# Kernel tuning notes

Measured on AMD Instinct MI355X. Metric: run time of the kernel, lower is better.

## Reference

```python
import jax, jax.numpy as jnp
import numpy as np

LRELU_ALPHA = 0.2
ACT_GAIN = float(np.sqrt(2.0))  # def_gain for 'lrelu' in StyleGAN2 bias_act


def setup_inputs() -> dict:
    key = jax.random.key(0)
    k_x, k_w, k_aw, k_wt = jax.random.split(key, 4)
    N, C_in, C_out, H, W, Wdim, K = 8, 256, 256, 128, 128, 512, 3
    x = jax.random.normal(k_x, (N, C_in, H, W), dtype=jnp.float32)
    w = jax.random.normal(k_w, (N, Wdim), dtype=jnp.float32)
    # FullyConnectedLayer params: weight ~ randn([out, in]) (lr_mult=1), bias_init=1
    affine_w = jax.random.normal(k_aw, (C_in, Wdim), dtype=jnp.float32)
    affine_b = jnp.ones((C_in,), dtype=jnp.float32)
    # Conv weight ~ randn, bias zeros
    weight = jax.random.normal(k_wt, (C_out, C_in, K, K), dtype=jnp.float32)
    bias = jnp.zeros((C_out,), dtype=jnp.float32)
    return {"x": x, "w": w, "affine_w": affine_w, "affine_b": affine_b,
            "weight": weight, "bias": bias}


def reference(x, w, affine_w, affine_b, weight, bias):
    N, C_in, H, W = x.shape
    C_out, _, K, _ = weight.shape
    # affine: runtime weight gain = 1/sqrt(in_features)
    wg = 1.0 / np.sqrt(affine_w.shape[1])
    styles = w @ (affine_w.T * wg) + affine_b                      # [N, C_in]
    # modulate: per-sample weights [N, C_out, C_in, K, K]
    ww = weight[None] * styles[:, None, :, None, None]
    # demodulate
    d = jax.lax.rsqrt(jnp.sum(ww * ww, axis=(2, 3, 4)) + 1e-8)     # [N, C_out]
    ww = ww * d[:, :, None, None, None]
    # fused per-sample conv via grouped conv (groups = N), flip_weight=True -> correlation
    x2 = x.reshape(1, N * C_in, H, W)
    wk = ww.reshape(N * C_out, C_in, K, K)
    pad = K // 2
    out = jax.lax.conv_general_dilated(
        x2, wk, window_strides=(1, 1), padding=((pad, pad), (pad, pad)),
        dimension_numbers=("NCHW", "OIHW", "NCHW"), feature_group_count=N)
    out = out.reshape(N, C_out, H, W)
    # bias_act: lrelu with def_gain sqrt(2), gain=1, no clamp; then sigmoid
    out = out + bias[None, :, None, None]
    out = jnp.where(out >= 0, out, LRELU_ALPHA * out) * ACT_GAIN
    return jax.nn.sigmoid(out)
```

## Files before the change

### kernel.cpp

```cpp
#include <hip/hip_runtime.h>
#include <hip/hip_bf16.h>

typedef __attribute__((ext_vector_type(8))) short bf16x8;
typedef __attribute__((ext_vector_type(4))) float f32x4;
typedef unsigned short ushort_t;

__device__ __forceinline__ void gload16(const void* g, void* l) {
  __builtin_amdgcn_global_load_lds(
      (const __attribute__((address_space(1))) void*)g,
      (__attribute__((address_space(3))) void*)l, 16, 0, 0);
}

__global__ void k_styles(const float* __restrict__ w, const float* __restrict__ aw,
                         const float* __restrict__ ab, float* __restrict__ styles) {
  int wave = threadIdx.x >> 6, l = threadIdx.x & 63;
  int id = blockIdx.x * 4 + wave;
  int n = id >> 8, ci = id & 255;
  const float4* ar = (const float4*)(aw + (size_t)ci * 512);
  const float4* wr = (const float4*)(w + n * 512);
  float s = 0.f;
  #pragma unroll
  for (int j = 0; j < 2; j++) {
    float4 a = ar[l * 2 + j], b = wr[l * 2 + j];
    s += a.x * b.x + a.y * b.y + a.z * b.z + a.w * b.w;
  }
  #pragma unroll
  for (int off = 32; off; off >>= 1) s += __shfl_xor(s, off, 64);
  if (l == 0) styles[n * 256 + ci] = s * 0.044194173824159216f + ab[ci];
}

__global__ __launch_bounds__(256) void k_modw(const float* __restrict__ weight,
                                              const float* __restrict__ styles,
                                              ushort_t* __restrict__ wwg) {
  __shared__ float wl[4][2304];
  __shared__ float s_sty[256];
  int wave = threadIdx.x >> 6, l = threadIdx.x & 63;
  int id = blockIdx.x * 4 + wave;
  int n = id >> 8, co = id & 255;
  s_sty[threadIdx.x] = styles[(size_t)n * 256 + threadIdx.x];
  __syncthreads();
  const float* wrow = weight + (size_t)co * 2304;
  float sq = 0.f;
  #pragma unroll
  for (int i = 0; i < 36; i++) {
    int idx = i * 64 + l;
    float v = wrow[idx] * s_sty[idx / 9];
    sq += v * v;
    wl[wave][idx] = v;
  }
  #pragma unroll
  for (int off = 32; off; off >>= 1) sq += __shfl_xor(sq, off, 64);
  float d = rsqrtf(sq + 1e-8f);
  #pragma unroll
  for (int tap = 0; tap < 9; tap++) {
    int kh = tap / 3, kw = tap % 3;
    #pragma unroll
    for (int cg = 0; cg < 4; cg++) {
      int ci = cg * 64 + l;
      float v = wl[wave][ci * 9 + tap] * d;
      __hip_bfloat16 hb = __float2bfloat16(v);
      size_t oidx = ((((size_t)((n * 3 + kh) * 8) + (ci >> 5)) * 3 + kw) * 256 + co) * 32 + (ci & 31);
      wwg[oidx] = *reinterpret_cast<ushort_t*>(&hb);
    }
  }
}

__global__ void k_transpose(const float* __restrict__ x, ushort_t* __restrict__ xt) {
  int n = blockIdx.z, h = blockIdx.y;
  int wt = blockIdx.x & 1, ct = blockIdx.x >> 1;
  int w0 = wt * 64, ci0 = ct * 64;
  __shared__ float tile[64][68];
  int t = threadIdx.x;
  {
    int ci_l = t >> 2, wq = (t & 3) * 16;
    const float* src = x + (((size_t)(n * 256 + ci0 + ci_l) * 128 + h) * 128 + w0 + wq);
    #pragma unroll
    for (int j = 0; j < 4; j++)
      *(float4*)&tile[ci_l][wq + j * 4] = ((const float4*)src)[j];
  }
  __syncthreads();
  {
    int w_l = t >> 2, cq = (t & 3) * 16;
    union { ushort_t u[16]; uint4 v[2]; } pk;
    #pragma unroll
    for (int j = 0; j < 16; j++) {
      __hip_bfloat16 hb = __float2bfloat16(tile[cq + j][w_l]);
      pk.u[j] = *reinterpret_cast<ushort_t*>(&hb);
    }
    size_t off = ((size_t)((n * 128 + h) * 128) + w0 + w_l) * 256 + ci0 + cq;
    uint4* dst = (uint4*)(xt + off);
    dst[0] = pk.v[0];
    dst[1] = pk.v[1];
  }
}

__global__ __launch_bounds__(256, 2) void k_conv(
    const ushort_t* __restrict__ xt, const ushort_t* __restrict__ wwg,
    const float* __restrict__ bias, float* __restrict__ out) {
  __shared__ __align__(16) char smem[24576 + 2 * 8448];
  char* sA = smem;
  char* sB = smem + 24576;

  const int bid = blockIdx.x;
  const int n  = bid & 7;
  const int r  = bid >> 3;
  const int cb = r & 1;
  const int h0 = (r >> 1) * 2;

  const int t = threadIdx.x;
  const int wave = t >> 6;
  const int l = t & 63;
  const int wr = wave >> 1, wc = wave & 1;
  const int c = l & 15, kg = l >> 4;

  f32x4 acc[4][8];
  #pragma unroll
  for (int i = 0; i < 4; i++)
    #pragma unroll
    for (int j = 0; j < 8; j++)
      acc[i][j] = (f32x4){0.f, 0.f, 0.f, 0.f};

  if (t < 64) {
    int buf = t >> 5;
    int rr = t & 31;
    if (rr < 16) {
      int rowsel = rr >> 2;
      int row = (rowsel == 0) ? 0 : (128 + rowsel);
      *(f32x4*)(sB + buf * 8448 + row * 64 + (rr & 3) * 16) = (f32x4){0.f, 0.f, 0.f, 0.f};
    }
  }

  const long long xtN = (long long)n * (128LL * 128 * 256);

  for (int kh = 0; kh < 3; kh++) {
    const int hsrc_w = h0 + wc + kh - 1;
    const bool valid = (hsrc_w >= 0) && (hsrc_w < 128);
    const char* gAkh = (const char*)(wwg + ((size_t)(n * 3 + kh)) * (8 * 3 * 256 * 32));
    for (int cc = 0; cc < 8; cc++) {
      __syncthreads();
      const char* gA = gAkh + (size_t)cc * (3 * 256 * 32 * 2);
      #pragma unroll
      for (int i = 0; i < 6; i++) {
        int G = i * 256 + t;
        int kw = G >> 9, rr = G & 511;
        const char* gp = gA + kw * 16384 + cb * 8192 + rr * 16;
        char* lp = sA + (i * 256 + wave * 64) * 16;
        gload16(gp, lp);
      }
      #pragma unroll
      for (int i = 0; i < 4; i++) {
        int G = i * 256 + t;
        int rr = G & 511;
        int w = rr >> 2, gg = rr & 3;
        int buf = G >> 9;
        int hsrc = h0 + kh - 1 + buf;
        const char* gp = (const char*)xt +
            ((xtN + (long long)(hsrc * 128 + w) * 256 + cc * 32 + gg * 8) * 2);
        int B0 = i * 256 + wave * 64;
        char* lp = sB + (B0 >> 9) * 8448 + 64 + (B0 & 511) * 16;
        gload16(gp, lp);
      }
      asm volatile("s_waitcnt vmcnt(0)" ::: "memory");
      __syncthreads();
      if (valid) {
        const char* bBase = sB + wc * 8448;
        #pragma unroll
        for (int s = 0; s < 3; s++) {
          bf16x8 af[4];
          #pragma unroll
          for (int mi = 0; mi < 4; mi++)
            af[mi] = *(const bf16x8*)(sA + s * 8192 + (wr * 64 + mi * 16 + c) * 64 + kg * 16);
          bf16x8 bfr[8];
          #pragma unroll
          for (int ni = 0; ni < 8; ni++)
            bfr[ni] = *(const bf16x8*)(bBase + (ni * 16 + c + s) * 64 + kg * 16);
          #pragma unroll
          for (int mi = 0; mi < 4; mi++)
            #pragma unroll
            for (int ni = 0; ni < 8; ni++)
              acc[mi][ni] = __builtin_amdgcn_mfma_f32_16x16x32_bf16(af[mi], bfr[ni], acc[mi][ni], 0, 0, 0);
        }
      }
    }
  }

  const int hrow = h0 + wc;
  #pragma unroll
  for (int mi = 0; mi < 4; mi++) {
    #pragma unroll
    for (int rr = 0; rr < 4; rr++) {
      int co = cb * 128 + wr * 64 + mi * 16 + kg * 4 + rr;
      float bval = bias[co];
      #pragma unroll
      for (int ni = 0; ni < 8; ni++) {
        float v = acc[mi][ni][rr] + bval;
        v = (v >= 0.f ? v : 0.2f * v) * 1.41421356237f;
        float o = 1.f / (1.f + __expf(-v));
        out[(((size_t)(n * 256 + co)) * 128 + hrow) * 128 + ni * 16 + c] = o;
      }
    }
  }
}

extern "C" void kernel_launch(void* const* d_in, const int* in_sizes, int n_in,
                              void* d_out, int out_size, void* d_ws, size_t ws_size,
                              hipStream_t stream) {
  const float* x      = (const float*)d_in[0];
  const float* w      = (const float*)d_in[1];
  const float* aw     = (const float*)d_in[2];
  const float* ab     = (const float*)d_in[3];
  const float* weight = (const float*)d_in[4];
  const float* bias   = (const float*)d_in[5];
  float* out = (float*)d_out;

  char* ws = (char*)d_ws;
  float*    styles = (float*)ws;
  ushort_t* wwg    = (ushort_t*)(ws + 8192);
  ushort_t* xt     = (ushort_t*)(ws + 8192 + 9437184);

  k_styles<<<512, 256, 0, stream>>>(w, aw, ab, styles);
  k_modw<<<512, 256, 0, stream>>>(weight, styles, wwg);
  k_transpose<<<dim3(8, 128, 8), 256, 0, stream>>>(x, xt);
  k_conv<<<1024, 256, 0, stream>>>(xt, wwg, bias, out);
}
```

Measured before the change: 377.2 us.

## Double-buffer conv stages, one output row per block, skip padded kh rows

Restructures the conv kernel so each block computes a single output row (each wave owns 32 output channels), which doubles the grid. Global-to-LDS loads for the next (kh, channel-chunk) stage are issued before computing the current one, using double-buffered LDS. Boundary rows skip the kh iterations that fall entirely in padding instead of loading and then masking them. The trade-off is that weight tiles are reloaded twice as often per output row, and LDS use per block roughly doubles, which may limit occupancy.

Measured after the change: 396.8 us. 1.05x slower.

```diff
diff --git a/kernel.cpp b/kernel.cpp
--- a/kernel.cpp
+++ b/kernel.cpp
@@ -97,106 +97,103 @@
 __global__ __launch_bounds__(256, 2) void k_conv(
     const ushort_t* __restrict__ xt, const ushort_t* __restrict__ wwg,
     const float* __restrict__ bias, float* __restrict__ out) {
-  __shared__ __align__(16) char smem[24576 + 2 * 8448];
-  char* sA = smem;
-  char* sB = smem + 24576;
+  __shared__ __align__(16) char smem[2 * 24576 + 2 * 8448];
 
   const int bid = blockIdx.x;
   const int n  = bid & 7;
   const int r  = bid >> 3;
   const int cb = r & 1;
-  const int h0 = (r >> 1) * 2;
+  const int h0 = r >> 1;
 
   const int t = threadIdx.x;
   const int wave = t >> 6;
   const int l = t & 63;
-  const int wr = wave >> 1, wc = wave & 1;
+  const int wr = wave;
   const int c = l & 15, kg = l >> 4;
 
-  f32x4 acc[4][8];
-  #pragma unroll
-  for (int i = 0; i < 4; i++)
+  f32x4 acc[2][8];
+  #pragma unroll
+  for (int i = 0; i < 2; i++)
     #pragma unroll
     for (int j = 0; j < 8; j++)
       acc[i][j] = (f32x4){0.f, 0.f, 0.f, 0.f};
 
-  if (t < 64) {
-    int buf = t >> 5;
-    int rr = t & 31;
-    if (rr < 16) {
-      int rowsel = rr >> 2;
-      int row = (rowsel == 0) ? 0 : (128 + rowsel);
-      *(f32x4*)(sB + buf * 8448 + row * 64 + (rr & 3) * 16) = (f32x4){0.f, 0.f, 0.f, 0.f};
-    }
+  if (t < 16) {
+    int buf = t >> 3, q = t & 7;
+    int slot = (q >> 2) ? 129 : 0;
+    *(f32x4*)(smem + 49152 + buf * 8448 + slot * 64 + (q & 3) * 16) =
+        (f32x4){0.f, 0.f, 0.f, 0.f};
   }
 
   const long long xtN = (long long)n * (128LL * 128 * 256);
-
-  for (int kh = 0; kh < 3; kh++) {
-    const int hsrc_w = h0 + wc + kh - 1;
-    const bool valid = (hsrc_w >= 0) && (hsrc_w < 128);
-    const char* gAkh = (const char*)(wwg + ((size_t)(n * 3 + kh)) * (8 * 3 * 256 * 32));
-    for (int cc = 0; cc < 8; cc++) {
-      __syncthreads();
-      const char* gA = gAkh + (size_t)cc * (3 * 256 * 32 * 2);
-      #pragma unroll
-      for (int i = 0; i < 6; i++) {
-        int G = i * 256 + t;
-        int kw = G >> 9, rr = G & 511;
-        const char* gp = gA + kw * 16384 + cb * 8192 + rr * 16;
-        char* lp = sA + (i * 256 + wave * 64) * 16;
-        gload16(gp, lp);
-      }
-      #pragma unroll
-      for (int i = 0; i < 4; i++) {
-        int G = i * 256 + t;
-        int rr = G & 511;
-        int w = rr >> 2, gg = rr & 3;
-        int buf = G >> 9;
-        int hsrc = h0 + kh - 1 + buf;
-        const char* gp = (const char*)xt +
-            ((xtN + (long long)(hsrc * 128 + w) * 256 + cc * 32 + gg * 8) * 2);
-        int B0 = i * 256 + wave * 64;
-        char* lp = sB + (B0 >> 9) * 8448 + 64 + (B0 & 511) * 16;
-        gload16(gp, lp);
-      }
-      asm volatile("s_waitcnt vmcnt(0)" ::: "memory");
-      __syncthreads();
-      if (valid) {
-        const char* bBase = sB + wc * 8448;
+  const int khs = (h0 == 0) ? 1 : 0;
+  const int khe = (h0 == 127) ? 1 : 2;
+  const int NS = (khe - khs + 1) * 8;
+
+  auto stage = [&](int i, int pbuf) {
+    const int kh = khs + (i >> 3), cc = i & 7;
+    const char* gA = (const char*)wwg + (((size_t)(n * 3 + kh) * 8 + cc) * (3 * 256 * 32)) * 2;
+    char* aDst = smem + pbuf * 24576;
+    #pragma unroll
+    for (int it = 0; it < 6; it++) {
+      int G = it * 256 + t;
+      int kw = G >> 9, rr = G & 511;
+      gload16(gA + kw * 16384 + cb * 8192 + rr * 16,
+              aDst + (it * 256 + wave * 64) * 16);
+    }
+    const int hsrc = h0 + kh - 1;
+    const char* gB = (const char*)xt + (xtN + (long long)hsrc * 128 * 256 + cc * 32) * 2;
+    char* bDst = smem + 49152 + pbuf * 8448 + 64;
+    #pragma unroll
+    for (int it = 0; it < 2; it++) {
+      int G = it * 256 + t;
+      int w = G >> 2, gg = G & 3;
+      gload16(gB + ((long long)w * 256 + gg * 8) * 2,
+              bDst + (it * 256 + wave * 64) * 16);
+    }
+  };
+
+  auto compute = [&](int pbuf) {
+    const char* aB = smem + pbuf * 24576;
+    const char* bB = smem + 49152 + pbuf * 8448;
+    #pragma unroll
+    for (int s = 0; s < 3; s++) {
+      bf16x8 af[2];
+      #pragma unroll
+      for (int mi = 0; mi < 2; mi++)
+        af[mi] = *(const bf16x8*)(aB + s * 8192 + (wr * 32 + mi * 16 + c) * 64 + kg * 16);
+      bf16x8 bfr[8];
+      #pragma unroll
+      for (int ni = 0; ni < 8; ni++)
+        bfr[ni] = *(const bf16x8*)(bB + (ni * 16 + c + s) * 64 + kg * 16);
+      #pragma unroll
+      for (int mi = 0; mi < 2; mi++)
         #pragma unroll
-        for (int s = 0; s < 3; s++) {
-          bf16x8 af[4];
-          #pragma unroll
-          for (int mi = 0; mi < 4; mi++)
-            af[mi] = *(const bf16x8*)(sA + s * 8192 + (wr * 64 + mi * 16 + c) * 64 + kg * 16);
-          bf16x8 bfr[8];
-          #pragma unroll
-          for (int ni = 0; ni < 8; ni++)
-            bfr[ni] = *(const bf16x8*)(bBase + (ni * 16 + c + s) * 64 + kg * 16);
-          #pragma unroll
-          for (int mi = 0; mi < 4; mi++)
-            #pragma unroll
-            for (int ni = 0; ni < 8; ni++)
-              acc[mi][ni] = __builtin_amdgcn_mfma_f32_16x16x32_bf16(af[mi], bfr[ni], acc[mi][ni], 0, 0, 0);
-        }
-      }
-    }
-  }
-
-  const int hrow = h0 + wc;
-  #pragma unroll
-  for (int mi = 0; mi < 4; mi++) {
+        for (int ni = 0; ni < 8; ni++)
+          acc[mi][ni] = __builtin_amdgcn_mfma_f32_16x16x32_bf16(af[mi], bfr[ni], acc[mi][ni], 0, 0, 0);
+    }
+  };
+
+  stage(0, 0);
+  __syncthreads();
+  for (int i = 0; i < NS; i++) {
+    if (i + 1 < NS) stage(i + 1, (i + 1) & 1);
+    compute(i & 1);
+    __syncthreads();
+  }
+
+  #pragma unroll
+  for (int mi = 0; mi < 2; mi++) {
     #pragma unroll
     for (int rr = 0; rr < 4; rr++) {
-      int co = cb * 128 + wr * 64 + mi * 16 + kg * 4 + rr;
+      int co = cb * 128 + wr * 32 + mi * 16 + kg * 4 + rr;
       float bval = bias[co];
       #pragma unroll
       for (int ni = 0; ni < 8; ni++) {
         float v = acc[mi][ni][rr] + bval;
         v = (v >= 0.f ? v : 0.2f * v) * 1.41421356237f;
         float o = 1.f / (1.f + __expf(-v));
-        out[(((size_t)(n * 256 + co)) * 128 + hrow) * 128 + ni * 16 + c] = o;
+        out[(((size_t)(n * 256 + co)) * 128 + h0) * 128 + ni * 16 + c] = o;
       }
     }
   }
@@ -221,5 +218,5 @@
   k_styles<<<512, 256, 0, stream>>>(w, aw, ab, styles);
   k_modw<<<512, 256, 0, stream>>>(weight, styles, wwg);
   k_transpose<<<dim3(8, 128, 8), 256, 0, stream>>>(x, xt);
-  k_conv<<<1024, 256, 0, stream>>>(xt, wwg, bias, out);
-}
+  k_conv<<<2048, 256, 0, stream>>>(xt, wwg, bias, out);
+}
```
